# Kernel tuning notes

Measured on AMD Instinct MI355X. Metric: run time of the kernel, lower is better.

## Reference

```python
import jax, jax.numpy as jnp
import numpy as np

N, E, G = 100000, 1600000, 1024
F_IN, D, C = 1, 32, 10

def _lin(key, fin, fout):
    return jax.random.normal(key, (fin, fout), jnp.float32) / np.sqrt(fin)

def setup_inputs() -> dict:
    key = jax.random.key(0)
    ks = jax.random.split(key, 32)
    inp = {}
    inp['x'] = jax.random.normal(ks[0], (N, F_IN), jnp.float32)
    inp['edge_index'] = jax.random.randint(ks[1], (2, E), 0, N)
    inp['batch'] = jnp.sort(jax.random.randint(ks[2], (N,), 0, G))
    inp['num_graphs'] = G
    # conv1: ResGatedGraphConv(F_IN -> D)
    inp['c1_Wk'] = _lin(ks[3], F_IN, D); inp['c1_bk'] = jnp.zeros((D,), jnp.float32)
    inp['c1_Wq'] = _lin(ks[4], F_IN, D); inp['c1_bq'] = jnp.zeros((D,), jnp.float32)
    inp['c1_Wv'] = _lin(ks[5], F_IN, D); inp['c1_bv'] = jnp.zeros((D,), jnp.float32)
    inp['c1_Wskip'] = _lin(ks[6], F_IN, D); inp['c1_b'] = jnp.zeros((D,), jnp.float32)
    # conv2: FiLMConv(D -> D), num_relations=1
    inp['c2_Wlin'] = _lin(ks[7], D, D)
    inp['c2_Wfilm'] = _lin(ks[8], D, 2 * D); inp['c2_bfilm'] = jnp.zeros((2 * D,), jnp.float32)
    inp['c2_Wls'] = _lin(ks[9], D, D)
    inp['c2_Wfs'] = _lin(ks[10], D, 2 * D)
    # conv3: ResGatedGraphConv(D -> D)
    inp['c3_Wk'] = _lin(ks[11], D, D); inp['c3_bk'] = jnp.zeros((D,), jnp.float32)
    inp['c3_Wq'] = _lin(ks[12], D, D); inp['c3_bq'] = jnp.zeros((D,), jnp.float32)
    inp['c3_Wv'] = _lin(ks[13], D, D); inp['c3_bv'] = jnp.zeros((D,), jnp.float32)
    inp['c3_Wskip'] = _lin(ks[14], D, D); inp['c3_b'] = jnp.zeros((D,), jnp.float32)
    # final classifier
    inp['lin_W'] = _lin(ks[15], D, C); inp['lin_b'] = jnp.zeros((C,), jnp.float32)
    return inp

def _res_gated(x, src, dst, Wk, bk, Wq, bq, Wv, bv, Wskip, b):
    # out_i = sum_{j->i} sigmoid(k_i + q_j) * v_j + W_skip x_i + b
    k = x @ Wk + bk
    q = x @ Wq + bq
    v = x @ Wv + bv
    msg = jax.nn.sigmoid(k[dst] + q[src]) * v[src]  # [E, D]
    agg = jax.ops.segment_sum(msg, dst, num_segments=x.shape[0])
    return agg + x @ Wskip + b

def _film(x, src, dst, Wlin, Wfilm, bfilm, Wls, Wfs):
    # skip path: relu(gamma_skip * (W_skip x) + beta_skip)
    bg_s = x @ Wfs                       # [N, 2D]
    beta_s, gamma_s = jnp.split(bg_s, 2, axis=-1)
    out = jax.nn.relu(gamma_s * (x @ Wls) + beta_s)
    # message path: relu(gamma_i * (W x_j) + beta_i), mean aggregation
    bg = x @ Wfilm + bfilm
    beta, gamma = jnp.split(bg, 2, axis=-1)
    xl = x @ Wlin
    msg = jax.nn.relu(gamma[dst] * xl[src] + beta[dst])  # [E, D]
    sums = jax.ops.segment_sum(msg, dst, num_segments=x.shape[0])
    cnt = jax.ops.segment_sum(jnp.ones((dst.shape[0], 1), x.dtype), dst, num_segments=x.shape[0])
    return out + sums / jnp.maximum(cnt, 1.0)

def reference(x, edge_index, batch, num_graphs,
              c1_Wk, c1_bk, c1_Wq, c1_bq, c1_Wv, c1_bv, c1_Wskip, c1_b,
              c2_Wlin, c2_Wfilm, c2_bfilm, c2_Wls, c2_Wfs,
              c3_Wk, c3_bk, c3_Wq, c3_bq, c3_Wv, c3_bv, c3_Wskip, c3_b,
              lin_W, lin_b):
    src, dst = edge_index[0], edge_index[1]
    h = _res_gated(x, src, dst, c1_Wk, c1_bk, c1_Wq, c1_bq, c1_Wv, c1_bv, c1_Wskip, c1_b)
    h = jax.nn.relu(h)
    h = _film(h, src, dst, c2_Wlin, c2_Wfilm, c2_bfilm, c2_Wls, c2_Wfs)
    h = jax.nn.relu(h)
    h = _res_gated(h, src, dst, c3_Wk, c3_bk, c3_Wq, c3_bq, c3_Wv, c3_bv, c3_Wskip, c3_b)
    # global mean pool over graphs
    sums = jax.ops.segment_sum(h, batch, num_segments=num_graphs)
    cnt = jax.ops.segment_sum(jnp.ones((h.shape[0], 1), h.dtype), batch, num_segments=num_graphs)
    g = sums / jnp.maximum(cnt, 1.0)
    # dropout is identity in eval mode
    return g @ lin_W + lin_b
```

## Files before the change

kernel.cpp:

```cpp
#include <hip/hip_runtime.h>

#define N_NODES 100000
#define N_EDGES 1600000
#define N_GRAPH 1024
#define NB      196
#define BCAP    10240
#define PEPT    16

typedef unsigned short u16;
typedef unsigned int   u32;

__device__ __forceinline__ float sigm(float z) { return 1.0f / (1.0f + __expf(-z)); }
__device__ __forceinline__ u16 f2bf(float f) {
    u32 u = __float_as_uint(f);
    u += 0x7FFFu + ((u >> 16) & 1u);
    return (u16)(u >> 16);
}
__device__ __forceinline__ float bf2f(u16 h) { return __uint_as_float(((u32)h) << 16); }

__global__ __launch_bounds__(256) void k_partition(const int* __restrict__ ei,
                                                   int* __restrict__ gcnt,
                                                   int* __restrict__ bucketed)
{
    __shared__ int lcnt[NB], gbase[NB], lcur[NB];
    int t = threadIdx.x;
    for (int i = t; i < NB; i += 256) { lcnt[i] = 0; lcur[i] = 0; }
    __syncthreads();

    int ebase = blockIdx.x * (256 * PEPT);
    int pk[PEPT], bk[PEPT];
#pragma unroll
    for (int r = 0; r < PEPT; r++) {
        int e = ebase + r * 256 + t;
        if (e < N_EDGES) {
            int d = ei[N_EDGES + e];
            int s = ei[e];
            int b = d >> 9;
            bk[r] = b;
            pk[r] = ((d & 511) << 17) | s;
            atomicAdd(&lcnt[b], 1);
        } else bk[r] = -1;
    }
    __syncthreads();
    for (int i = t; i < NB; i += 256) gbase[i] = atomicAdd(&gcnt[i], lcnt[i]);
    __syncthreads();
#pragma unroll
    for (int r = 0; r < PEPT; r++) {
        if (bk[r] >= 0) {
            int b = bk[r];
            int pos = gbase[b] + atomicAdd(&lcur[b], 1);
            bucketed[b * BCAP + pos] = pk[r];
        }
    }
}

__global__ __launch_bounds__(256) void k_bscan(const int* __restrict__ gcnt,
                                               int* __restrict__ base)
{
    __shared__ int s[256];
    int t = threadIdx.x;
    int v = (t < NB) ? gcnt[t] : 0;
    s[t] = v;
    __syncthreads();
#pragma unroll
    for (int off = 1; off < 256; off <<= 1) {
        int u = (t >= off) ? s[t - off] : 0;
        __syncthreads();
        s[t] += u;
        __syncthreads();
    }
    base[t] = s[t] - v;
}

__global__ __launch_bounds__(512) void k_place(const int* __restrict__ bucketed,
                                               const int* __restrict__ gcnt,
                                               const int* __restrict__ base,
                                               int* __restrict__ csr,
                                               int* __restrict__ starts,
                                               int* __restrict__ cnt)
{
    __shared__ int scnt[512], sexc[512], scur[512];
    int b = blockIdx.x, t = threadIdx.x;
    int ecnt = gcnt[b];
    int ebase = base[b];
    const int* bp = bucketed + b * BCAP;

    scnt[t] = 0; scur[t] = 0;
    __syncthreads();
    for (int e = t; e < ecnt; e += 512) atomicAdd(&scnt[bp[e] >> 17], 1);
    __syncthreads();
    int v = scnt[t];
    sexc[t] = v;
    __syncthreads();
#pragma unroll
    for (int off = 1; off < 512; off <<= 1) {
        int u = (t >= off) ? sexc[t - off] : 0;
        __syncthreads();
        sexc[t] += u;
        __syncthreads();
    }
    int excl = sexc[t] - v;
    __syncthreads();
    sexc[t] = excl;
    __syncthreads();

    int node = b * 512 + t;
    if (node < N_NODES) { starts[node] = ebase + excl; cnt[node] = v; }

    for (int e = t; e < ecnt; e += 512) {
        int p = bp[e];
        int ld = p >> 17;
        int pos = ebase + sexc[ld] + atomicAdd(&scur[ld], 1);
        csr[pos] = p & 0x1FFFF;
    }
}

__global__ __launch_bounds__(256) void k_gath1(
    const float* __restrict__ x, const int* __restrict__ csr_src,
    const int* __restrict__ starts, const int* __restrict__ cnt,
    const float* __restrict__ Wk, const float* __restrict__ bk,
    const float* __restrict__ Wq, const float* __restrict__ bq,
    const float* __restrict__ Wv, const float* __restrict__ bv,
    const float* __restrict__ Wskip, const float* __restrict__ b,
    float* __restrict__ h1)
{
    int tid = blockIdx.x * 256 + threadIdx.x;
    if (tid >= N_NODES * 8) return;
    int i = tid >> 3, l = tid & 7;

    float xd = x[i];
    float4 wk = ((const float4*)Wk)[l], bk4 = ((const float4*)bk)[l];
    float4 wq = ((const float4*)Wq)[l], bq4 = ((const float4*)bq)[l];
    float4 wv = ((const float4*)Wv)[l], bv4 = ((const float4*)bv)[l];
    float4 kk = make_float4(fmaf(xd, wk.x, bk4.x), fmaf(xd, wk.y, bk4.y),
                            fmaf(xd, wk.z, bk4.z), fmaf(xd, wk.w, bk4.w));

    int base = starts[i], deg = cnt[i];
    float4 a0 = make_float4(0.f, 0.f, 0.f, 0.f);
    float4 a1 = make_float4(0.f, 0.f, 0.f, 0.f);
    int e = 0;
    for (; e + 1 < deg; e += 2) {
        int s0 = csr_src[base + e];
        int s1 = csr_src[base + e + 1];
        float x0 = x[s0], x1 = x[s1];
        a0.x += sigm(kk.x + fmaf(x0, wq.x, bq4.x)) * fmaf(x0, wv.x, bv4.x);
        a0.y += sigm(kk.y + fmaf(x0, wq.y, bq4.y)) * fmaf(x0, wv.y, bv4.y);
        a0.z += sigm(kk.z + fmaf(x0, wq.z, bq4.z)) * fmaf(x0, wv.z, bv4.z);
        a0.w += sigm(kk.w + fmaf(x0, wq.w, bq4.w)) * fmaf(x0, wv.w, bv4.w);
        a1.x += sigm(kk.x + fmaf(x1, wq.x, bq4.x)) * fmaf(x1, wv.x, bv4.x);
        a1.y += sigm(kk.y + fmaf(x1, wq.y, bq4.y)) * fmaf(x1, wv.y, bv4.y);
        a1.z += sigm(kk.z + fmaf(x1, wq.z, bq4.z)) * fmaf(x1, wv.z, bv4.z);
        a1.w += sigm(kk.w + fmaf(x1, wq.w, bq4.w)) * fmaf(x1, wv.w, bv4.w);
    }
    if (e < deg) {
        int s0 = csr_src[base + e];
        float x0 = x[s0];
        a0.x += sigm(kk.x + fmaf(x0, wq.x, bq4.x)) * fmaf(x0, wv.x, bv4.x);
        a0.y += sigm(kk.y + fmaf(x0, wq.y, bq4.y)) * fmaf(x0, wv.y, bv4.y);
        a0.z += sigm(kk.z + fmaf(x0, wq.z, bq4.z)) * fmaf(x0, wv.z, bv4.z);
        a0.w += sigm(kk.w + fmaf(x0, wq.w, bq4.w)) * fmaf(x0, wv.w, bv4.w);
    }
    float4 ws4 = ((const float4*)Wskip)[l];
    float4 bb4 = ((const float4*)b)[l];
    float4 o = make_float4(a0.x + a1.x + fmaf(xd, ws4.x, bb4.x),
                           a0.y + a1.y + fmaf(xd, ws4.y, bb4.y),
                           a0.z + a1.z + fmaf(xd, ws4.z, bb4.z),
                           a0.w + a1.w + fmaf(xd, ws4.w, bb4.w));
    ((float4*)(h1 + (size_t)i * 32))[l] = o;
}

__device__ __forceinline__ float4 dot4(const float* __restrict__ h,
                                       const float* __restrict__ Wcol, int stride)
{
    float4 a = make_float4(0.f, 0.f, 0.f, 0.f);
#pragma unroll
    for (int k = 0; k < 32; k++) {
        float4 w = *(const float4*)(Wcol + k * stride);
        float hk = h[k];
        a.x = fmaf(hk, w.x, a.x);
        a.y = fmaf(hk, w.y, a.y);
        a.z = fmaf(hk, w.z, a.z);
        a.w = fmaf(hk, w.w, a.w);
    }
    return a;
}

__global__ __launch_bounds__(256) void k_node2(
    const float* __restrict__ h1,
    const float* __restrict__ Wlin, const float* __restrict__ Wfilm,
    const float* __restrict__ bfilm, const float* __restrict__ Wls,
    const float* __restrict__ Wfs,
    float* __restrict__ skip2, float* __restrict__ bg2, u16* __restrict__ xlb)
{
    __shared__ float sWlin[32 * 32], sWfilm[32 * 64], sWls[32 * 32], sWfs[32 * 64];
    int t = threadIdx.x;
    for (int idx = t; idx < 1024; idx += 256) sWlin[idx] = Wlin[idx];
    for (int idx = t; idx < 2048; idx += 256) sWfilm[idx] = Wfilm[idx];
    for (int idx = t; idx < 1024; idx += 256) sWls[idx] = Wls[idx];
    for (int idx = t; idx < 2048; idx += 256) sWfs[idx] = Wfs[idx];
    __syncthreads();

    int tid = blockIdx.x * 256 + t;
    if (tid >= N_NODES * 8) return;
    int i = tid >> 3, l = tid & 7;

    float h[32];
    const float4* hp = (const float4*)(h1 + (size_t)i * 32);
#pragma unroll
    for (int j = 0; j < 8; j++) {
        float4 v = hp[j];
        h[4 * j + 0] = fmaxf(v.x, 0.f);
        h[4 * j + 1] = fmaxf(v.y, 0.f);
        h[4 * j + 2] = fmaxf(v.z, 0.f);
        h[4 * j + 3] = fmaxf(v.w, 0.f);
    }

    float4 bs = dot4(h, sWfs + l * 4, 64);
    float4 gs = dot4(h, sWfs + 32 + l * 4, 64);
    float4 ls = dot4(h, sWls + l * 4, 32);
    float4 sk = make_float4(fmaxf(fmaf(gs.x, ls.x, bs.x), 0.f),
                            fmaxf(fmaf(gs.y, ls.y, bs.y), 0.f),
                            fmaxf(fmaf(gs.z, ls.z, bs.z), 0.f),
                            fmaxf(fmaf(gs.w, ls.w, bs.w), 0.f));
    ((float4*)(skip2 + (size_t)i * 32))[l] = sk;

    float4 bf0 = ((const float4*)bfilm)[l * 2];
    float4 bf1 = ((const float4*)bfilm)[l * 2 + 1];
    float4 f0 = dot4(h, sWfilm + l * 8, 64);
    float4 f1 = dot4(h, sWfilm + l * 8 + 4, 64);
    f0.x += bf0.x; f0.y += bf0.y; f0.z += bf0.z; f0.w += bf0.w;
    f1.x += bf1.x; f1.y += bf1.y; f1.z += bf1.z; f1.w += bf1.w;
    float4* bgp = (float4*)(bg2 + (size_t)i * 64);
    bgp[l * 2] = f0;
    bgp[l * 2 + 1] = f1;

    float4 xo = dot4(h, sWlin + l * 4, 32);
    ushort4 xp;
    xp.x = f2bf(xo.x); xp.y = f2bf(xo.y); xp.z = f2bf(xo.z); xp.w = f2bf(xo.w);
    ((ushort4*)xlb)[(size_t)i * 8 + l] = xp;
}

__global__ __launch_bounds__(256) void k_gath2(
    const int* __restrict__ csr_src, const int* __restrict__ starts,
    const int* __restrict__ cnt,
    const float* __restrict__ bg2, const u16* __restrict__ xlb,
    const float* __restrict__ skip2, float* __restrict__ h2)
{
    int tid = blockIdx.x * 256 + threadIdx.x;
    if (tid >= N_NODES * 8) return;
    int i = tid >> 3, l = tid & 7;

    float4 be = ((const float4*)(bg2 + (size_t)i * 64))[l];
    float4 ga = ((const float4*)(bg2 + (size_t)i * 64 + 32))[l];

    int base = starts[i], deg = cnt[i];
    float4 a0 = make_float4(0.f, 0.f, 0.f, 0.f);
    float4 a1 = make_float4(0.f, 0.f, 0.f, 0.f);
    int e = 0;
    for (; e + 1 < deg; e += 2) {
        int s0 = csr_src[base + e];
        int s1 = csr_src[base + e + 1];
        ushort4 u = ((const ushort4*)xlb)[(size_t)s0 * 8 + l];
        ushort4 w = ((const ushort4*)xlb)[(size_t)s1 * 8 + l];
        a0.x += fmaxf(fmaf(ga.x, bf2f(u.x), be.x), 0.f);
        a0.y += fmaxf(fmaf(ga.y, bf2f(u.y), be.y), 0.f);
        a0.z += fmaxf(fmaf(ga.z, bf2f(u.z), be.z), 0.f);
        a0.w += fmaxf(fmaf(ga.w, bf2f(u.w), be.w), 0.f);
        a1.x += fmaxf(fmaf(ga.x, bf2f(w.x), be.x), 0.f);
        a1.y += fmaxf(fmaf(ga.y, bf2f(w.y), be.y), 0.f);
        a1.z += fmaxf(fmaf(ga.z, bf2f(w.z), be.z), 0.f);
        a1.w += fmaxf(fmaf(ga.w, bf2f(w.w), be.w), 0.f);
    }
    if (e < deg) {
        int s0 = csr_src[base + e];
        ushort4 u = ((const ushort4*)xlb)[(size_t)s0 * 8 + l];
        a0.x += fmaxf(fmaf(ga.x, bf2f(u.x), be.x), 0.f);
        a0.y += fmaxf(fmaf(ga.y, bf2f(u.y), be.y), 0.f);
        a0.z += fmaxf(fmaf(ga.z, bf2f(u.z), be.z), 0.f);
        a0.w += fmaxf(fmaf(ga.w, bf2f(u.w), be.w), 0.f);
    }
    float inv = 1.0f / fmaxf((float)deg, 1.0f);
    float4 sk = ((const float4*)(skip2 + (size_t)i * 32))[l];
    float4 o = make_float4(fmaxf(fmaf(a0.x + a1.x, inv, sk.x), 0.f),
                           fmaxf(fmaf(a0.y + a1.y, inv, sk.y), 0.f),
                           fmaxf(fmaf(a0.z + a1.z, inv, sk.z), 0.f),
                           fmaxf(fmaf(a0.w + a1.w, inv, sk.w), 0.f));
    ((float4*)(h2 + (size_t)i * 32))[l] = o;
}

__global__ __launch_bounds__(256) void k_node3(
    const float* __restrict__ h2,
    const float* __restrict__ Wk, const float* __restrict__ bk,
    const float* __restrict__ Wq, const float* __restrict__ bq,
    const float* __restrict__ Wv, const float* __restrict__ bv,
    const float* __restrict__ Wskip, const float* __restrict__ b,
    float* __restrict__ k3, u16* __restrict__ qvb, float* __restrict__ acc3)
{
    __shared__ float sWk[1024], sWq[1024], sWv[1024], sWs[1024];
    int t = threadIdx.x;
    for (int idx = t; idx < 1024; idx += 256) {
        sWk[idx] = Wk[idx];
        sWq[idx] = Wq[idx];
        sWv[idx] = Wv[idx];
        sWs[idx] = Wskip[idx];
    }
    __syncthreads();

    int tid = blockIdx.x * 256 + t;
    if (tid >= N_NODES * 8) return;
    int i = tid >> 3, l = tid & 7;

    float h[32];
    const float4* hp = (const float4*)(h2 + (size_t)i * 32);
#pragma unroll
    for (int j = 0; j < 8; j++) {
        float4 v = hp[j];
        h[4 * j + 0] = v.x; h[4 * j + 1] = v.y;
        h[4 * j + 2] = v.z; h[4 * j + 3] = v.w;
    }

    float4 bk4 = ((const float4*)bk)[l];
    float4 bq4 = ((const float4*)bq)[l];
    float4 bv4 = ((const float4*)bv)[l];
    float4 bb4 = ((const float4*)b)[l];

    float4 kk = dot4(h, sWk + l * 4, 32);
    kk.x += bk4.x; kk.y += bk4.y; kk.z += bk4.z; kk.w += bk4.w;
    ((float4*)(k3 + (size_t)i * 32))[l] = kk;

    float4 qq = dot4(h, sWq + l * 4, 32);
    qq.x += bq4.x; qq.y += bq4.y; qq.z += bq4.z; qq.w += bq4.w;
    float4 vv = dot4(h, sWv + l * 4, 32);
    vv.x += bv4.x; vv.y += bv4.y; vv.z += bv4.z; vv.w += bv4.w;

    uint4 pk;
    pk.x = (u32)f2bf(qq.x) | ((u32)f2bf(qq.y) << 16);
    pk.y = (u32)f2bf(qq.z) | ((u32)f2bf(qq.w) << 16);
    pk.z = (u32)f2bf(vv.x) | ((u32)f2bf(vv.y) << 16);
    pk.w = (u32)f2bf(vv.z) | ((u32)f2bf(vv.w) << 16);
    ((uint4*)qvb)[(size_t)i * 8 + l] = pk;

    float4 ss = dot4(h, sWs + l * 4, 32);
    ss.x += bb4.x; ss.y += bb4.y; ss.z += bb4.z; ss.w += bb4.w;
    ((float4*)(acc3 + (size_t)i * 32))[l] = ss;
}

__global__ __launch_bounds__(256) void k_gath3(
    const int* __restrict__ csr_src, const int* __restrict__ starts,
    const int* __restrict__ cnt,
    const float* __restrict__ k3, const u16* __restrict__ qvb,
    float* __restrict__ acc3)
{
    int tid = blockIdx.x * 256 + threadIdx.x;
    if (tid >= N_NODES * 8) return;
    int i = tid >> 3, l = tid & 7;

    float4 kk = ((const float4*)(k3 + (size_t)i * 32))[l];
    int base = starts[i], deg = cnt[i];
    float4 a0 = make_float4(0.f, 0.f, 0.f, 0.f);
    float4 a1 = make_float4(0.f, 0.f, 0.f, 0.f);
    int e = 0;
    for (; e + 1 < deg; e += 2) {
        int s0 = csr_src[base + e];
        int s1 = csr_src[base + e + 1];
        uint4 p0 = ((const uint4*)qvb)[(size_t)s0 * 8 + l];
        uint4 p1 = ((const uint4*)qvb)[(size_t)s1 * 8 + l];
        a0.x += sigm(kk.x + bf2f((u16)p0.x)) * bf2f((u16)p0.z);
        a0.y += sigm(kk.y + bf2f((u16)(p0.x >> 16))) * bf2f((u16)(p0.z >> 16));
        a0.z += sigm(kk.z + bf2f((u16)p0.y)) * bf2f((u16)p0.w);
        a0.w += sigm(kk.w + bf2f((u16)(p0.y >> 16))) * bf2f((u16)(p0.w >> 16));
        a1.x += sigm(kk.x + bf2f((u16)p1.x)) * bf2f((u16)p1.z);
        a1.y += sigm(kk.y + bf2f((u16)(p1.x >> 16))) * bf2f((u16)(p1.z >> 16));
        a1.z += sigm(kk.z + bf2f((u16)p1.y)) * bf2f((u16)p1.w);
        a1.w += sigm(kk.w + bf2f((u16)(p1.y >> 16))) * bf2f((u16)(p1.w >> 16));
    }
    if (e < deg) {
        int s0 = csr_src[base + e];
        uint4 p0 = ((const uint4*)qvb)[(size_t)s0 * 8 + l];
        a0.x += sigm(kk.x + bf2f((u16)p0.x)) * bf2f((u16)p0.z);
        a0.y += sigm(kk.y + bf2f((u16)(p0.x >> 16))) * bf2f((u16)(p0.z >> 16));
        a0.z += sigm(kk.z + bf2f((u16)p0.y)) * bf2f((u16)p0.w);
        a0.w += sigm(kk.w + bf2f((u16)(p0.y >> 16))) * bf2f((u16)(p0.w >> 16));
    }
    float4* op = (float4*)(acc3 + (size_t)i * 32) + l;
    float4 cur = *op;
    cur.x += a0.x + a1.x;
    cur.y += a0.y + a1.y;
    cur.z += a0.z + a1.z;
    cur.w += a0.w + a1.w;
    *op = cur;
}

__global__ __launch_bounds__(256) void k_gstart(const int* __restrict__ batch,
                                                int* __restrict__ gstart)
{
    int g = blockIdx.x * 256 + threadIdx.x;
    if (g > N_GRAPH) return;
    int lo = 0, hi = N_NODES;
    while (lo < hi) {
        int mid = (lo + hi) >> 1;
        if (batch[mid] < g) lo = mid + 1; else hi = mid;
    }
    gstart[g] = lo;
}

__global__ __launch_bounds__(256) void k_pool(
    const float* __restrict__ h3, const int* __restrict__ gstart,
    float* __restrict__ gmean)
{
    int tid = blockIdx.x * 256 + threadIdx.x;
    int g = tid >> 6;
    if (g >= N_GRAPH) return;
    int lane = tid & 63;
    int sub = lane >> 3, fg = lane & 7;
    int gs = gstart[g], ge = gstart[g + 1];

    float4 a = make_float4(0.f, 0.f, 0.f, 0.f);
    for (int j = gs + sub; j < ge; j += 8) {
        float4 v = ((const float4*)(h3 + (size_t)j * 32))[fg];
        a.x += v.x; a.y += v.y; a.z += v.z; a.w += v.w;
    }
#pragma unroll
    for (int off = 8; off < 64; off <<= 1) {
        a.x += __shfl_xor(a.x, off);
        a.y += __shfl_xor(a.y, off);
        a.z += __shfl_xor(a.z, off);
        a.w += __shfl_xor(a.w, off);
    }
    if (sub == 0) {
        float inv = 1.0f / fmaxf((float)(ge - gs), 1.0f);
        a.x *= inv; a.y *= inv; a.z *= inv; a.w *= inv;
        ((float4*)(gmean + (size_t)g * 32))[fg] = a;
    }
}

__global__ __launch_bounds__(256) void k_final(
    const float* __restrict__ gmean,
    const float* __restrict__ linW, const float* __restrict__ linb,
    float* __restrict__ out)
{
    int tid = blockIdx.x * 256 + threadIdx.x;
    if (tid >= N_GRAPH * 10) return;
    int g = tid / 10, c = tid % 10;
    const float* gr = gmean + (size_t)g * 32;
    float a = 0.f;
#pragma unroll
    for (int k = 0; k < 32; k++) a = fmaf(gr[k], linW[k * 10 + c], a);
    out[tid] = a + linb[c];
}

extern "C" void kernel_launch(void* const* d_in, const int* in_sizes, int n_in,
                              void* d_out, int out_size, void* d_ws, size_t ws_size,
                              hipStream_t stream)
{
    const float* x      = (const float*)d_in[0];
    const int*   ei     = (const int*)d_in[1];
    const int*   batch  = (const int*)d_in[2];
    const float* c1_Wk   = (const float*)d_in[4];
    const float* c1_bk   = (const float*)d_in[5];
    const float* c1_Wq   = (const float*)d_in[6];
    const float* c1_bq   = (const float*)d_in[7];
    const float* c1_Wv   = (const float*)d_in[8];
    const float* c1_bv   = (const float*)d_in[9];
    const float* c1_Wsk  = (const float*)d_in[10];
    const float* c1_b    = (const float*)d_in[11];
    const float* c2_Wlin = (const float*)d_in[12];
    const float* c2_Wfilm= (const float*)d_in[13];
    const float* c2_bfilm= (const float*)d_in[14];
    const float* c2_Wls  = (const float*)d_in[15];
    const float* c2_Wfs  = (const float*)d_in[16];
    const float* c3_Wk   = (const float*)d_in[17];
    const float* c3_bk   = (const float*)d_in[18];
    const float* c3_Wq   = (const float*)d_in[19];
    const float* c3_bq   = (const float*)d_in[20];
    const float* c3_Wv   = (const float*)d_in[21];
    const float* c3_bv   = (const float*)d_in[22];
    const float* c3_Wsk  = (const float*)d_in[23];
    const float* c3_b    = (const float*)d_in[24];
    const float* lin_W   = (const float*)d_in[25];
    const float* lin_b   = (const float*)d_in[26];
    float* out = (float*)d_out;

    const size_t N = N_NODES;

    int* gcnt    = (int*)d_ws;
    int* bbase   = gcnt + 256;
    int* igstart = bbase + 256;
    int* bucketed= igstart + 1056;
    int* icsr    = bucketed + NB * BCAP;
    int* istarts = icsr + N_EDGES;
    int* icnt    = istarts + N;
    float* fbase = (float*)(icnt + N);
    float* h1    = fbase;
    float* skip2 = h1 + N * 32;
    float* bg2   = skip2 + N * 32;
    u16*   xlb   = (u16*)(bg2 + N * 64);
    float* gmean = (float*)(xlb + N * 32);

    hipMemsetAsync(gcnt, 0, 256 * sizeof(int), stream);

    const int TB = 256;
    int gPart  = (N_EDGES + 256 * PEPT - 1) / (256 * PEPT);
    int gNode8 = (N_NODES * 8 + TB - 1) / TB;
    int gFin   = (N_GRAPH * 10 + TB - 1) / TB;

    k_partition<<<gPart, TB, 0, stream>>>(ei, gcnt, bucketed);
    k_bscan<<<1, 256, 0, stream>>>(gcnt, bbase);
    k_place<<<NB, 512, 0, stream>>>(bucketed, gcnt, bbase, icsr, istarts, icnt);
    k_gstart<<<5, TB, 0, stream>>>(batch, igstart);

    k_gath1<<<gNode8, TB, 0, stream>>>(x, icsr, istarts, icnt,
                                       c1_Wk, c1_bk, c1_Wq, c1_bq,
                                       c1_Wv, c1_bv, c1_Wsk, c1_b, h1);
    k_node2<<<gNode8, TB, 0, stream>>>(h1, c2_Wlin, c2_Wfilm, c2_bfilm,
                                       c2_Wls, c2_Wfs, skip2, bg2, xlb);
    float* h2 = h1;
    k_gath2<<<gNode8, TB, 0, stream>>>(icsr, istarts, icnt, bg2, xlb, skip2, h2);
    float* k3   = skip2;
    u16*   qvb  = (u16*)bg2;
    float* acc3 = bg2 + N * 32;
    k_node3<<<gNode8, TB, 0, stream>>>(h2, c3_Wk, c3_bk, c3_Wq, c3_bq,
                                       c3_Wv, c3_bv, c3_Wsk, c3_b,
                                       k3, qvb, acc3);
    k_gath3<<<gNode8, TB, 0, stream>>>(icsr, istarts, icnt, k3, qvb, acc3);
    k_pool<<<256, TB, 0, stream>>>(acc3, igstart, gmean);
    k_final<<<gFin, TB, 0, stream>>>(gmean, lin_W, lin_b, out);
}
```

Measured before the change: 338.4 us.

## Fuse per-node transforms into gather kernels and degree-sort node processing order

Splits the node-wise transforms so that only the source-side projections (xl, q/v) are precomputed. The destination-side projections (FiLM beta/gamma, skip, k) are now computed inside the gather kernels, which removes writing and re-reading the skip2, bg2, k3 and acc3 intermediates. It also builds a per-block degree-binned permutation in k_place so the gather kernels process nodes grouped by similar degree, which reduces divergence within a wavefront. The cost is recomputing small matvecs inside the gathers, extra shared-memory weight loads per block, and an indirection through perm that scatters the per-node reads and writes.

```diff
diff --git a/kernel.cpp b/kernel.cpp
--- a/kernel.cpp
+++ b/kernel.cpp
@@ -77,9 +77,10 @@
                                                const int* __restrict__ base,
                                                int* __restrict__ csr,
                                                int* __restrict__ starts,
-                                               int* __restrict__ cnt)
-{
-    __shared__ int scnt[512], sexc[512], scur[512];
+                                               int* __restrict__ cnt,
+                                               int* __restrict__ perm)
+{
+    __shared__ int scnt[512], sexc[512], scur[512], dbin[64];
     int b = blockIdx.x, t = threadIdx.x;
     int ecnt = gcnt[b];
     int ebase = base[b];
@@ -113,11 +114,30 @@
         int pos = ebase + sexc[ld] + atomicAdd(&scur[ld], 1);
         csr[pos] = p & 0x1FFFF;
     }
+
+    __syncthreads();
+    if (t < 64) dbin[t] = 0;
+    __syncthreads();
+    int nvalid = N_NODES - b * 512;
+    if (nvalid > 512) nvalid = 512;
+    int mybin = (t < nvalid) ? (v < 63 ? v : 63) : -1;
+    if (mybin >= 0) atomicAdd(&dbin[mybin], 1);
+    __syncthreads();
+    if (t == 0) {
+        int acc = 0;
+        for (int i = 0; i < 64; i++) { int c = dbin[i]; dbin[i] = acc; acc += c; }
+    }
+    __syncthreads();
+    if (mybin >= 0) {
+        int pos = atomicAdd(&dbin[mybin], 1);
+        perm[b * 512 + pos] = node;
+    }
 }
 
 __global__ __launch_bounds__(256) void k_gath1(
     const float* __restrict__ x, const int* __restrict__ csr_src,
     const int* __restrict__ starts, const int* __restrict__ cnt,
+    const int* __restrict__ perm,
     const float* __restrict__ Wk, const float* __restrict__ bk,
     const float* __restrict__ Wq, const float* __restrict__ bq,
     const float* __restrict__ Wv, const float* __restrict__ bv,
@@ -126,7 +146,7 @@
 {
     int tid = blockIdx.x * 256 + threadIdx.x;
     if (tid >= N_NODES * 8) return;
-    int i = tid >> 3, l = tid & 7;
+    int i = perm[tid >> 3], l = tid & 7;
 
     float xd = x[i];
     float4 wk = ((const float4*)Wk)[l], bk4 = ((const float4*)bk)[l];
@@ -185,16 +205,45 @@
     return a;
 }
 
-__global__ __launch_bounds__(256) void k_node2(
-    const float* __restrict__ h1,
-    const float* __restrict__ Wlin, const float* __restrict__ Wfilm,
-    const float* __restrict__ bfilm, const float* __restrict__ Wls,
-    const float* __restrict__ Wfs,
-    float* __restrict__ skip2, float* __restrict__ bg2, u16* __restrict__ xlb)
-{
-    __shared__ float sWlin[32 * 32], sWfilm[32 * 64], sWls[32 * 32], sWfs[32 * 64];
+__global__ __launch_bounds__(256) void k_xl(
+    const float* __restrict__ h1, const float* __restrict__ Wlin,
+    u16* __restrict__ xlb)
+{
+    __shared__ float sWlin[1024];
     int t = threadIdx.x;
     for (int idx = t; idx < 1024; idx += 256) sWlin[idx] = Wlin[idx];
+    __syncthreads();
+
+    int tid = blockIdx.x * 256 + t;
+    if (tid >= N_NODES * 8) return;
+    int i = tid >> 3, l = tid & 7;
+
+    float h[32];
+    const float4* hp = (const float4*)(h1 + (size_t)i * 32);
+#pragma unroll
+    for (int j = 0; j < 8; j++) {
+        float4 v = hp[j];
+        h[4 * j + 0] = fmaxf(v.x, 0.f);
+        h[4 * j + 1] = fmaxf(v.y, 0.f);
+        h[4 * j + 2] = fmaxf(v.z, 0.f);
+        h[4 * j + 3] = fmaxf(v.w, 0.f);
+    }
+    float4 xo = dot4(h, sWlin + l * 4, 32);
+    ushort4 xp;
+    xp.x = f2bf(xo.x); xp.y = f2bf(xo.y); xp.z = f2bf(xo.z); xp.w = f2bf(xo.w);
+    ((ushort4*)xlb)[(size_t)i * 8 + l] = xp;
+}
+
+__global__ __launch_bounds__(256) void k_gath2f(
+    const int* __restrict__ csr_src, const int* __restrict__ starts,
+    const int* __restrict__ cnt, const int* __restrict__ perm,
+    const float* __restrict__ h1, const u16* __restrict__ xlb,
+    const float* __restrict__ Wfilm, const float* __restrict__ bfilm,
+    const float* __restrict__ Wls, const float* __restrict__ Wfs,
+    float* __restrict__ h2)
+{
+    __shared__ float sWfilm[2048], sWls[1024], sWfs[2048];
+    int t = threadIdx.x;
     for (int idx = t; idx < 2048; idx += 256) sWfilm[idx] = Wfilm[idx];
     for (int idx = t; idx < 1024; idx += 256) sWls[idx] = Wls[idx];
     for (int idx = t; idx < 2048; idx += 256) sWfs[idx] = Wfs[idx];
@@ -202,7 +251,7 @@
 
     int tid = blockIdx.x * 256 + t;
     if (tid >= N_NODES * 8) return;
-    int i = tid >> 3, l = tid & 7;
+    int i = perm[tid >> 3], l = tid & 7;
 
     float h[32];
     const float4* hp = (const float4*)(h1 + (size_t)i * 32);
@@ -222,36 +271,13 @@
                             fmaxf(fmaf(gs.y, ls.y, bs.y), 0.f),
                             fmaxf(fmaf(gs.z, ls.z, bs.z), 0.f),
                             fmaxf(fmaf(gs.w, ls.w, bs.w), 0.f));
-    ((float4*)(skip2 + (size_t)i * 32))[l] = sk;
-
-    float4 bf0 = ((const float4*)bfilm)[l * 2];
-    float4 bf1 = ((const float4*)bfilm)[l * 2 + 1];
-    float4 f0 = dot4(h, sWfilm + l * 8, 64);
-    float4 f1 = dot4(h, sWfilm + l * 8 + 4, 64);
-    f0.x += bf0.x; f0.y += bf0.y; f0.z += bf0.z; f0.w += bf0.w;
-    f1.x += bf1.x; f1.y += bf1.y; f1.z += bf1.z; f1.w += bf1.w;
-    float4* bgp = (float4*)(bg2 + (size_t)i * 64);
-    bgp[l * 2] = f0;
-    bgp[l * 2 + 1] = f1;
-
-    float4 xo = dot4(h, sWlin + l * 4, 32);
-    ushort4 xp;
-    xp.x = f2bf(xo.x); xp.y = f2bf(xo.y); xp.z = f2bf(xo.z); xp.w = f2bf(xo.w);
-    ((ushort4*)xlb)[(size_t)i * 8 + l] = xp;
-}
-
-__global__ __launch_bounds__(256) void k_gath2(
-    const int* __restrict__ csr_src, const int* __restrict__ starts,
-    const int* __restrict__ cnt,
-    const float* __restrict__ bg2, const u16* __restrict__ xlb,
-    const float* __restrict__ skip2, float* __restrict__ h2)
-{
-    int tid = blockIdx.x * 256 + threadIdx.x;
-    if (tid >= N_NODES * 8) return;
-    int i = tid >> 3, l = tid & 7;
-
-    float4 be = ((const float4*)(bg2 + (size_t)i * 64))[l];
-    float4 ga = ((const float4*)(bg2 + (size_t)i * 64 + 32))[l];
+
+    float4 bf = ((const float4*)bfilm)[l];
+    float4 gf = ((const float4*)bfilm)[8 + l];
+    float4 be = dot4(h, sWfilm + l * 4, 64);
+    float4 ga = dot4(h, sWfilm + 32 + l * 4, 64);
+    be.x += bf.x; be.y += bf.y; be.z += bf.z; be.w += bf.w;
+    ga.x += gf.x; ga.y += gf.y; ga.z += gf.z; ga.w += gf.w;
 
     int base = starts[i], deg = cnt[i];
     float4 a0 = make_float4(0.f, 0.f, 0.f, 0.f);
@@ -280,7 +306,6 @@
         a0.w += fmaxf(fmaf(ga.w, bf2f(u.w), be.w), 0.f);
     }
     float inv = 1.0f / fmaxf((float)deg, 1.0f);
-    float4 sk = ((const float4*)(skip2 + (size_t)i * 32))[l];
     float4 o = make_float4(fmaxf(fmaf(a0.x + a1.x, inv, sk.x), 0.f),
                            fmaxf(fmaf(a0.y + a1.y, inv, sk.y), 0.f),
                            fmaxf(fmaf(a0.z + a1.z, inv, sk.z), 0.f),
@@ -288,22 +313,15 @@
     ((float4*)(h2 + (size_t)i * 32))[l] = o;
 }
 
-__global__ __launch_bounds__(256) void k_node3(
+__global__ __launch_bounds__(256) void k_qv(
     const float* __restrict__ h2,
-    const float* __restrict__ Wk, const float* __restrict__ bk,
     const float* __restrict__ Wq, const float* __restrict__ bq,
     const float* __restrict__ Wv, const float* __restrict__ bv,
-    const float* __restrict__ Wskip, const float* __restrict__ b,
-    float* __restrict__ k3, u16* __restrict__ qvb, float* __restrict__ acc3)
-{
-    __shared__ float sWk[1024], sWq[1024], sWv[1024], sWs[1024];
+    u16* __restrict__ qvb)
+{
+    __shared__ float sWq[1024], sWv[1024];
     int t = threadIdx.x;
-    for (int idx = t; idx < 1024; idx += 256) {
-        sWk[idx] = Wk[idx];
-        sWq[idx] = Wq[idx];
-        sWv[idx] = Wv[idx];
-        sWs[idx] = Wskip[idx];
-    }
+    for (int idx = t; idx < 1024; idx += 256) { sWq[idx] = Wq[idx]; sWv[idx] = Wv[idx]; }
     __syncthreads();
 
     int tid = blockIdx.x * 256 + t;
@@ -318,16 +336,8 @@
         h[4 * j + 0] = v.x; h[4 * j + 1] = v.y;
         h[4 * j + 2] = v.z; h[4 * j + 3] = v.w;
     }
-
-    float4 bk4 = ((const float4*)bk)[l];
     float4 bq4 = ((const float4*)bq)[l];
     float4 bv4 = ((const float4*)bv)[l];
-    float4 bb4 = ((const float4*)b)[l];
-
-    float4 kk = dot4(h, sWk + l * 4, 32);
-    kk.x += bk4.x; kk.y += bk4.y; kk.z += bk4.z; kk.w += bk4.w;
-    ((float4*)(k3 + (size_t)i * 32))[l] = kk;
-
     float4 qq = dot4(h, sWq + l * 4, 32);
     qq.x += bq4.x; qq.y += bq4.y; qq.z += bq4.z; qq.w += bq4.w;
     float4 vv = dot4(h, sWv + l * 4, 32);
@@ -339,23 +349,40 @@
     pk.z = (u32)f2bf(vv.x) | ((u32)f2bf(vv.y) << 16);
     pk.w = (u32)f2bf(vv.z) | ((u32)f2bf(vv.w) << 16);
     ((uint4*)qvb)[(size_t)i * 8 + l] = pk;
-
+}
+
+__global__ __launch_bounds__(256) void k_gath3f(
+    const int* __restrict__ csr_src, const int* __restrict__ starts,
+    const int* __restrict__ cnt, const int* __restrict__ perm,
+    const float* __restrict__ h2, const u16* __restrict__ qvb,
+    const float* __restrict__ Wk, const float* __restrict__ bk,
+    const float* __restrict__ Wskip, const float* __restrict__ b,
+    float* __restrict__ h3)
+{
+    __shared__ float sWk[1024], sWs[1024];
+    int t = threadIdx.x;
+    for (int idx = t; idx < 1024; idx += 256) { sWk[idx] = Wk[idx]; sWs[idx] = Wskip[idx]; }
+    __syncthreads();
+
+    int tid = blockIdx.x * 256 + t;
+    if (tid >= N_NODES * 8) return;
+    int i = perm[tid >> 3], l = tid & 7;
+
+    float h[32];
+    const float4* hp = (const float4*)(h2 + (size_t)i * 32);
+#pragma unroll
+    for (int j = 0; j < 8; j++) {
+        float4 v = hp[j];
+        h[4 * j + 0] = v.x; h[4 * j + 1] = v.y;
+        h[4 * j + 2] = v.z; h[4 * j + 3] = v.w;
+    }
+    float4 bk4 = ((const float4*)bk)[l];
+    float4 bb4 = ((const float4*)b)[l];
+    float4 kk = dot4(h, sWk + l * 4, 32);
+    kk.x += bk4.x; kk.y += bk4.y; kk.z += bk4.z; kk.w += bk4.w;
     float4 ss = dot4(h, sWs + l * 4, 32);
     ss.x += bb4.x; ss.y += bb4.y; ss.z += bb4.z; ss.w += bb4.w;
-    ((float4*)(acc3 + (size_t)i * 32))[l] = ss;
-}
-
-__global__ __launch_bounds__(256) void k_gath3(
-    const int* __restrict__ csr_src, const int* __restrict__ starts,
-    const int* __restrict__ cnt,
-    const float* __restrict__ k3, const u16* __restrict__ qvb,
-    float* __restrict__ acc3)
-{
-    int tid = blockIdx.x * 256 + threadIdx.x;
-    if (tid >= N_NODES * 8) return;
-    int i = tid >> 3, l = tid & 7;
-
-    float4 kk = ((const float4*)(k3 + (size_t)i * 32))[l];
+
     int base = starts[i], deg = cnt[i];
     float4 a0 = make_float4(0.f, 0.f, 0.f, 0.f);
     float4 a1 = make_float4(0.f, 0.f, 0.f, 0.f);
@@ -382,13 +409,9 @@
         a0.z += sigm(kk.z + bf2f((u16)p0.y)) * bf2f((u16)p0.w);
         a0.w += sigm(kk.w + bf2f((u16)(p0.y >> 16))) * bf2f((u16)(p0.w >> 16));
     }
-    float4* op = (float4*)(acc3 + (size_t)i * 32) + l;
-    float4 cur = *op;
-    cur.x += a0.x + a1.x;
-    cur.y += a0.y + a1.y;
-    cur.z += a0.z + a1.z;
-    cur.w += a0.w + a1.w;
-    *op = cur;
+    float4 o = make_float4(ss.x + a0.x + a1.x, ss.y + a0.y + a1.y,
+                           ss.z + a0.z + a1.z, ss.w + a0.w + a1.w);
+    ((float4*)(h3 + (size_t)i * 32))[l] = o;
 }
 
 __global__ __launch_bounds__(256) void k_gstart(const int* __restrict__ batch,
@@ -490,12 +513,12 @@
     int* icsr    = bucketed + NB * BCAP;
     int* istarts = icsr + N_EDGES;
     int* icnt    = istarts + N;
-    float* fbase = (float*)(icnt + N);
-    float* h1    = fbase;
-    float* skip2 = h1 + N * 32;
-    float* bg2   = skip2 + N * 32;
-    u16*   xlb   = (u16*)(bg2 + N * 64);
-    float* gmean = (float*)(xlb + N * 32);
+    int* iperm   = icnt + N;
+    float* h1    = (float*)(iperm + N);
+    float* h2    = h1 + N * 32;
+    u16*   xlb   = (u16*)(h2 + N * 32);
+    u16*   qvb   = xlb + N * 32;
+    float* gmean = (float*)(qvb + N * 64);
 
     hipMemsetAsync(gcnt, 0, 256 * sizeof(int), stream);
 
@@ -506,23 +529,19 @@
 
     k_partition<<<gPart, TB, 0, stream>>>(ei, gcnt, bucketed);
     k_bscan<<<1, 256, 0, stream>>>(gcnt, bbase);
-    k_place<<<NB, 512, 0, stream>>>(bucketed, gcnt, bbase, icsr, istarts, icnt);
+    k_place<<<NB, 512, 0, stream>>>(bucketed, gcnt, bbase, icsr, istarts, icnt, iperm);
     k_gstart<<<5, TB, 0, stream>>>(batch, igstart);
 
-    k_gath1<<<gNode8, TB, 0, stream>>>(x, icsr, istarts, icnt,
+    k_gath1<<<gNode8, TB, 0, stream>>>(x, icsr, istarts, icnt, iperm,
                                        c1_Wk, c1_bk, c1_Wq, c1_bq,
                                        c1_Wv, c1_bv, c1_Wsk, c1_b, h1);
-    k_node2<<<gNode8, TB, 0, stream>>>(h1, c2_Wlin, c2_Wfilm, c2_bfilm,
-                                       c2_Wls, c2_Wfs, skip2, bg2, xlb);
-    float* h2 = h1;
-    k_gath2<<<gNode8, TB, 0, stream>>>(icsr, istarts, icnt, bg2, xlb, skip2, h2);
-    float* k3   = skip2;
-    u16*   qvb  = (u16*)bg2;
-    float* acc3 = bg2 + N * 32;
-    k_node3<<<gNode8, TB, 0, stream>>>(h2, c3_Wk, c3_bk, c3_Wq, c3_bq,
-                                       c3_Wv, c3_bv, c3_Wsk, c3_b,
-                                       k3, qvb, acc3);
-    k_gath3<<<gNode8, TB, 0, stream>>>(icsr, istarts, icnt, k3, qvb, acc3);
-    k_pool<<<256, TB, 0, stream>>>(acc3, igstart, gmean);
+    k_xl<<<gNode8, TB, 0, stream>>>(h1, c2_Wlin, xlb);
+    k_gath2f<<<gNode8, TB, 0, stream>>>(icsr, istarts, icnt, iperm, h1, xlb,
+                                        c2_Wfilm, c2_bfilm, c2_Wls, c2_Wfs, h2);
+    k_qv<<<gNode8, TB, 0, stream>>>(h2, c3_Wq, c3_bq, c3_Wv, c3_bv, qvb);
+    float* h3 = h1;
+    k_gath3f<<<gNode8, TB, 0, stream>>>(icsr, istarts, icnt, iperm, h2, qvb,
+                                        c3_Wk, c3_bk, c3_Wsk, c3_b, h3);
+    k_pool<<<256, TB, 0, stream>>>(h3, igstart, gmean);
     k_final<<<gFin, TB, 0, stream>>>(gmean, lin_W, lin_b, out);
 }
```

Result: slower. 510.4 us (+50.8%).

## Factor sigmoid into per-node exponentials and unroll gather loops by four

Applied to the files above, without the earlier changes.

Rewrites sigmoid(k_i+q_j) as 1/(1+exp(-k_i)*exp(-q_j)), so the exponentials are computed once per node and each edge costs only an FMA plus a hardware reciprocal. A new pre-kernel for layer 1 precomputes packed bf16 exp(-q) and v per node, and layer 3's node kernel now stores exp(-k) and exp(-q). The gather loops in all three layers are unrolled to four edges to keep more loads in flight. In exchange there is an extra kernel launch, layer 1 now reads 16-byte bf16 rows per edge instead of a scalar x, and exp(-q) in bf16 can overflow or lose precision for large activations.

```diff
diff --git a/kernel.cpp b/kernel.cpp
--- a/kernel.cpp
+++ b/kernel.cpp
@@ -10,13 +10,13 @@
 typedef unsigned short u16;
 typedef unsigned int   u32;
 
-__device__ __forceinline__ float sigm(float z) { return 1.0f / (1.0f + __expf(-z)); }
 __device__ __forceinline__ u16 f2bf(float f) {
     u32 u = __float_as_uint(f);
     u += 0x7FFFu + ((u >> 16) & 1u);
     return (u16)(u >> 16);
 }
 __device__ __forceinline__ float bf2f(u16 h) { return __uint_as_float(((u32)h) << 16); }
+__device__ __forceinline__ float rcpf(float x) { return __builtin_amdgcn_rcpf(x); }
 
 __global__ __launch_bounds__(256) void k_partition(const int* __restrict__ ei,
                                                    int* __restrict__ gcnt,
@@ -115,12 +115,45 @@
     }
 }
 
+__global__ __launch_bounds__(256) void k_pre1(
+    const float* __restrict__ x,
+    const float* __restrict__ Wq, const float* __restrict__ bq,
+    const float* __restrict__ Wv, const float* __restrict__ bv,
+    u32* __restrict__ eqv1)
+{
+    int tid = blockIdx.x * 256 + threadIdx.x;
+    if (tid >= N_NODES * 8) return;
+    int i = tid >> 3, l = tid & 7;
+    float xv = x[i];
+    float4 wq = ((const float4*)Wq)[l], bq4 = ((const float4*)bq)[l];
+    float4 wv = ((const float4*)Wv)[l], bv4 = ((const float4*)bv)[l];
+    float e0 = __expf(-fmaf(xv, wq.x, bq4.x));
+    float e1 = __expf(-fmaf(xv, wq.y, bq4.y));
+    float e2 = __expf(-fmaf(xv, wq.z, bq4.z));
+    float e3 = __expf(-fmaf(xv, wq.w, bq4.w));
+    float v0 = fmaf(xv, wv.x, bv4.x);
+    float v1 = fmaf(xv, wv.y, bv4.y);
+    float v2 = fmaf(xv, wv.z, bv4.z);
+    float v3 = fmaf(xv, wv.w, bv4.w);
+    uint4 pk;
+    pk.x = (u32)f2bf(e0) | ((u32)f2bf(e1) << 16);
+    pk.y = (u32)f2bf(e2) | ((u32)f2bf(e3) << 16);
+    pk.z = (u32)f2bf(v0) | ((u32)f2bf(v1) << 16);
+    pk.w = (u32)f2bf(v2) | ((u32)f2bf(v3) << 16);
+    ((uint4*)eqv1)[(size_t)i * 8 + l] = pk;
+}
+
+#define EDGE_ACC(P, ACC)                                                        \
+    ACC.x += bf2f((u16)(P.z)) * rcpf(fmaf(ek.x, bf2f((u16)(P.x)), 1.0f));       \
+    ACC.y += bf2f((u16)(P.z >> 16)) * rcpf(fmaf(ek.y, bf2f((u16)(P.x >> 16)), 1.0f)); \
+    ACC.z += bf2f((u16)(P.w)) * rcpf(fmaf(ek.z, bf2f((u16)(P.y)), 1.0f));       \
+    ACC.w += bf2f((u16)(P.w >> 16)) * rcpf(fmaf(ek.w, bf2f((u16)(P.y >> 16)), 1.0f));
+
 __global__ __launch_bounds__(256) void k_gath1(
     const float* __restrict__ x, const int* __restrict__ csr_src,
     const int* __restrict__ starts, const int* __restrict__ cnt,
+    const u32* __restrict__ eqv1,
     const float* __restrict__ Wk, const float* __restrict__ bk,
-    const float* __restrict__ Wq, const float* __restrict__ bq,
-    const float* __restrict__ Wv, const float* __restrict__ bv,
     const float* __restrict__ Wskip, const float* __restrict__ b,
     float* __restrict__ h1)
 {
@@ -130,35 +163,32 @@
 
     float xd = x[i];
     float4 wk = ((const float4*)Wk)[l], bk4 = ((const float4*)bk)[l];
-    float4 wq = ((const float4*)Wq)[l], bq4 = ((const float4*)bq)[l];
-    float4 wv = ((const float4*)Wv)[l], bv4 = ((const float4*)bv)[l];
-    float4 kk = make_float4(fmaf(xd, wk.x, bk4.x), fmaf(xd, wk.y, bk4.y),
-                            fmaf(xd, wk.z, bk4.z), fmaf(xd, wk.w, bk4.w));
+    float4 ek;
+    ek.x = __expf(-fmaf(xd, wk.x, bk4.x));
+    ek.y = __expf(-fmaf(xd, wk.y, bk4.y));
+    ek.z = __expf(-fmaf(xd, wk.z, bk4.z));
+    ek.w = __expf(-fmaf(xd, wk.w, bk4.w));
 
     int base = starts[i], deg = cnt[i];
+    const uint4* qv = (const uint4*)eqv1;
     float4 a0 = make_float4(0.f, 0.f, 0.f, 0.f);
     float4 a1 = make_float4(0.f, 0.f, 0.f, 0.f);
     int e = 0;
-    for (; e + 1 < deg; e += 2) {
+    for (; e + 3 < deg; e += 4) {
         int s0 = csr_src[base + e];
         int s1 = csr_src[base + e + 1];
-        float x0 = x[s0], x1 = x[s1];
-        a0.x += sigm(kk.x + fmaf(x0, wq.x, bq4.x)) * fmaf(x0, wv.x, bv4.x);
-        a0.y += sigm(kk.y + fmaf(x0, wq.y, bq4.y)) * fmaf(x0, wv.y, bv4.y);
-        a0.z += sigm(kk.z + fmaf(x0, wq.z, bq4.z)) * fmaf(x0, wv.z, bv4.z);
-        a0.w += sigm(kk.w + fmaf(x0, wq.w, bq4.w)) * fmaf(x0, wv.w, bv4.w);
-        a1.x += sigm(kk.x + fmaf(x1, wq.x, bq4.x)) * fmaf(x1, wv.x, bv4.x);
-        a1.y += sigm(kk.y + fmaf(x1, wq.y, bq4.y)) * fmaf(x1, wv.y, bv4.y);
-        a1.z += sigm(kk.z + fmaf(x1, wq.z, bq4.z)) * fmaf(x1, wv.z, bv4.z);
-        a1.w += sigm(kk.w + fmaf(x1, wq.w, bq4.w)) * fmaf(x1, wv.w, bv4.w);
-    }
-    if (e < deg) {
+        int s2 = csr_src[base + e + 2];
+        int s3 = csr_src[base + e + 3];
+        uint4 p0 = qv[(size_t)s0 * 8 + l];
+        uint4 p1 = qv[(size_t)s1 * 8 + l];
+        uint4 p2 = qv[(size_t)s2 * 8 + l];
+        uint4 p3 = qv[(size_t)s3 * 8 + l];
+        EDGE_ACC(p0, a0) EDGE_ACC(p1, a1) EDGE_ACC(p2, a0) EDGE_ACC(p3, a1)
+    }
+    for (; e < deg; e++) {
         int s0 = csr_src[base + e];
-        float x0 = x[s0];
-        a0.x += sigm(kk.x + fmaf(x0, wq.x, bq4.x)) * fmaf(x0, wv.x, bv4.x);
-        a0.y += sigm(kk.y + fmaf(x0, wq.y, bq4.y)) * fmaf(x0, wv.y, bv4.y);
-        a0.z += sigm(kk.z + fmaf(x0, wq.z, bq4.z)) * fmaf(x0, wv.z, bv4.z);
-        a0.w += sigm(kk.w + fmaf(x0, wq.w, bq4.w)) * fmaf(x0, wv.w, bv4.w);
+        uint4 p0 = qv[(size_t)s0 * 8 + l];
+        EDGE_ACC(p0, a0)
     }
     float4 ws4 = ((const float4*)Wskip)[l];
     float4 bb4 = ((const float4*)b)[l];
@@ -192,7 +222,7 @@
     const float* __restrict__ Wfs,
     float* __restrict__ skip2, float* __restrict__ bg2, u16* __restrict__ xlb)
 {
-    __shared__ float sWlin[32 * 32], sWfilm[32 * 64], sWls[32 * 32], sWfs[32 * 64];
+    __shared__ float sWlin[1024], sWfilm[2048], sWls[1024], sWfs[2048];
     int t = threadIdx.x;
     for (int idx = t; idx < 1024; idx += 256) sWlin[idx] = Wlin[idx];
     for (int idx = t; idx < 2048; idx += 256) sWfilm[idx] = Wfilm[idx];
@@ -240,6 +270,12 @@
     ((ushort4*)xlb)[(size_t)i * 8 + l] = xp;
 }
 
+#define EDGE_ACC2(U, ACC)                                   \
+    ACC.x += fmaxf(fmaf(ga.x, bf2f(U.x), be.x), 0.f);       \
+    ACC.y += fmaxf(fmaf(ga.y, bf2f(U.y), be.y), 0.f);       \
+    ACC.z += fmaxf(fmaf(ga.z, bf2f(U.z), be.z), 0.f);       \
+    ACC.w += fmaxf(fmaf(ga.w, bf2f(U.w), be.w), 0.f);
+
 __global__ __launch_bounds__(256) void k_gath2(
     const int* __restrict__ csr_src, const int* __restrict__ starts,
     const int* __restrict__ cnt,
@@ -254,32 +290,27 @@
     float4 ga = ((const float4*)(bg2 + (size_t)i * 64 + 32))[l];
 
     int base = starts[i], deg = cnt[i];
+    const ushort4* xp = (const ushort4*)xlb;
     float4 a0 = make_float4(0.f, 0.f, 0.f, 0.f);
     float4 a1 = make_float4(0.f, 0.f, 0.f, 0.f);
     int e = 0;
-    for (; e + 1 < deg; e += 2) {
+    for (; e + 3 < deg; e += 4) {
         int s0 = csr_src[base + e];
         int s1 = csr_src[base + e + 1];
-        ushort4 u = ((const ushort4*)xlb)[(size_t)s0 * 8 + l];
-        ushort4 w = ((const ushort4*)xlb)[(size_t)s1 * 8 + l];
-        a0.x += fmaxf(fmaf(ga.x, bf2f(u.x), be.x), 0.f);
-        a0.y += fmaxf(fmaf(ga.y, bf2f(u.y), be.y), 0.f);
-        a0.z += fmaxf(fmaf(ga.z, bf2f(u.z), be.z), 0.f);
-        a0.w += fmaxf(fmaf(ga.w, bf2f(u.w), be.w), 0.f);
-        a1.x += fmaxf(fmaf(ga.x, bf2f(w.x), be.x), 0.f);
-        a1.y += fmaxf(fmaf(ga.y, bf2f(w.y), be.y), 0.f);
-        a1.z += fmaxf(fmaf(ga.z, bf2f(w.z), be.z), 0.f);
-        a1.w += fmaxf(fmaf(ga.w, bf2f(w.w), be.w), 0.f);
-    }
-    if (e < deg) {
+        int s2 = csr_src[base + e + 2];
+        int s3 = csr_src[base + e + 3];
+        ushort4 u0 = xp[(size_t)s0 * 8 + l];
+        ushort4 u1 = xp[(size_t)s1 * 8 + l];
+        ushort4 u2 = xp[(size_t)s2 * 8 + l];
+        ushort4 u3 = xp[(size_t)s3 * 8 + l];
+        EDGE_ACC2(u0, a0) EDGE_ACC2(u1, a1) EDGE_ACC2(u2, a0) EDGE_ACC2(u3, a1)
+    }
+    for (; e < deg; e++) {
         int s0 = csr_src[base + e];
-        ushort4 u = ((const ushort4*)xlb)[(size_t)s0 * 8 + l];
-        a0.x += fmaxf(fmaf(ga.x, bf2f(u.x), be.x), 0.f);
-        a0.y += fmaxf(fmaf(ga.y, bf2f(u.y), be.y), 0.f);
-        a0.z += fmaxf(fmaf(ga.z, bf2f(u.z), be.z), 0.f);
-        a0.w += fmaxf(fmaf(ga.w, bf2f(u.w), be.w), 0.f);
-    }
-    float inv = 1.0f / fmaxf((float)deg, 1.0f);
+        ushort4 u0 = xp[(size_t)s0 * 8 + l];
+        EDGE_ACC2(u0, a0)
+    }
+    float inv = rcpf(fmaxf((float)deg, 1.0f));
     float4 sk = ((const float4*)(skip2 + (size_t)i * 32))[l];
     float4 o = make_float4(fmaxf(fmaf(a0.x + a1.x, inv, sk.x), 0.f),
                            fmaxf(fmaf(a0.y + a1.y, inv, sk.y), 0.f),
@@ -294,7 +325,7 @@
     const float* __restrict__ Wq, const float* __restrict__ bq,
     const float* __restrict__ Wv, const float* __restrict__ bv,
     const float* __restrict__ Wskip, const float* __restrict__ b,
-    float* __restrict__ k3, u16* __restrict__ qvb, float* __restrict__ acc3)
+    float* __restrict__ ek3, u32* __restrict__ qvb, float* __restrict__ acc3)
 {
     __shared__ float sWk[1024], sWq[1024], sWv[1024], sWs[1024];
     int t = threadIdx.x;
@@ -325,17 +356,24 @@
     float4 bb4 = ((const float4*)b)[l];
 
     float4 kk = dot4(h, sWk + l * 4, 32);
-    kk.x += bk4.x; kk.y += bk4.y; kk.z += bk4.z; kk.w += bk4.w;
-    ((float4*)(k3 + (size_t)i * 32))[l] = kk;
+    float4 ekv;
+    ekv.x = __expf(-(kk.x + bk4.x));
+    ekv.y = __expf(-(kk.y + bk4.y));
+    ekv.z = __expf(-(kk.z + bk4.z));
+    ekv.w = __expf(-(kk.w + bk4.w));
+    ((float4*)(ek3 + (size_t)i * 32))[l] = ekv;
 
     float4 qq = dot4(h, sWq + l * 4, 32);
-    qq.x += bq4.x; qq.y += bq4.y; qq.z += bq4.z; qq.w += bq4.w;
     float4 vv = dot4(h, sWv + l * 4, 32);
+    float eq0 = __expf(-(qq.x + bq4.x));
+    float eq1 = __expf(-(qq.y + bq4.y));
+    float eq2 = __expf(-(qq.z + bq4.z));
+    float eq3 = __expf(-(qq.w + bq4.w));
     vv.x += bv4.x; vv.y += bv4.y; vv.z += bv4.z; vv.w += bv4.w;
 
     uint4 pk;
-    pk.x = (u32)f2bf(qq.x) | ((u32)f2bf(qq.y) << 16);
-    pk.y = (u32)f2bf(qq.z) | ((u32)f2bf(qq.w) << 16);
+    pk.x = (u32)f2bf(eq0) | ((u32)f2bf(eq1) << 16);
+    pk.y = (u32)f2bf(eq2) | ((u32)f2bf(eq3) << 16);
     pk.z = (u32)f2bf(vv.x) | ((u32)f2bf(vv.y) << 16);
     pk.w = (u32)f2bf(vv.z) | ((u32)f2bf(vv.w) << 16);
     ((uint4*)qvb)[(size_t)i * 8 + l] = pk;
@@ -348,39 +386,34 @@
 __global__ __launch_bounds__(256) void k_gath3(
     const int* __restrict__ csr_src, const int* __restrict__ starts,
     const int* __restrict__ cnt,
-    const float* __restrict__ k3, const u16* __restrict__ qvb,
+    const float* __restrict__ ek3, const u32* __restrict__ qvb,
     float* __restrict__ acc3)
 {
     int tid = blockIdx.x * 256 + threadIdx.x;
     if (tid >= N_NODES * 8) return;
     int i = tid >> 3, l = tid & 7;
 
-    float4 kk = ((const float4*)(k3 + (size_t)i * 32))[l];
+    float4 ek = ((const float4*)(ek3 + (size_t)i * 32))[l];
     int base = starts[i], deg = cnt[i];
+    const uint4* qv = (const uint4*)qvb;
     float4 a0 = make_float4(0.f, 0.f, 0.f, 0.f);
     float4 a1 = make_float4(0.f, 0.f, 0.f, 0.f);
     int e = 0;
-    for (; e + 1 < deg; e += 2) {
+    for (; e + 3 < deg; e += 4) {
         int s0 = csr_src[base + e];
         int s1 = csr_src[base + e + 1];
-        uint4 p0 = ((const uint4*)qvb)[(size_t)s0 * 8 + l];
-        uint4 p1 = ((const uint4*)qvb)[(size_t)s1 * 8 + l];
-        a0.x += sigm(kk.x + bf2f((u16)p0.x)) * bf2f((u16)p0.z);
-        a0.y += sigm(kk.y + bf2f((u16)(p0.x >> 16))) * bf2f((u16)(p0.z >> 16));
-        a0.z += sigm(kk.z + bf2f((u16)p0.y)) * bf2f((u16)p0.w);
-        a0.w += sigm(kk.w + bf2f((u16)(p0.y >> 16))) * bf2f((u16)(p0.w >> 16));
-        a1.x += sigm(kk.x + bf2f((u16)p1.x)) * bf2f((u16)p1.z);
-        a1.y += sigm(kk.y + bf2f((u16)(p1.x >> 16))) * bf2f((u16)(p1.z >> 16));
-        a1.z += sigm(kk.z + bf2f((u16)p1.y)) * bf2f((u16)p1.w);
-        a1.w += sigm(kk.w + bf2f((u16)(p1.y >> 16))) * bf2f((u16)(p1.w >> 16));
-    }
-    if (e < deg) {
+        int s2 = csr_src[base + e + 2];
+        int s3 = csr_src[base + e + 3];
+        uint4 p0 = qv[(size_t)s0 * 8 + l];
+        uint4 p1 = qv[(size_t)s1 * 8 + l];
+        uint4 p2 = qv[(size_t)s2 * 8 + l];
+        uint4 p3 = qv[(size_t)s3 * 8 + l];
+        EDGE_ACC(p0, a0) EDGE_ACC(p1, a1) EDGE_ACC(p2, a0) EDGE_ACC(p3, a1)
+    }
+    for (; e < deg; e++) {
         int s0 = csr_src[base + e];
-        uint4 p0 = ((const uint4*)qvb)[(size_t)s0 * 8 + l];
-        a0.x += sigm(kk.x + bf2f((u16)p0.x)) * bf2f((u16)p0.z);
-        a0.y += sigm(kk.y + bf2f((u16)(p0.x >> 16))) * bf2f((u16)(p0.z >> 16));
-        a0.z += sigm(kk.z + bf2f((u16)p0.y)) * bf2f((u16)p0.w);
-        a0.w += sigm(kk.w + bf2f((u16)(p0.y >> 16))) * bf2f((u16)(p0.w >> 16));
+        uint4 p0 = qv[(size_t)s0 * 8 + l];
+        EDGE_ACC(p0, a0)
     }
     float4* op = (float4*)(acc3 + (size_t)i * 32) + l;
     float4 cur = *op;
@@ -490,12 +523,12 @@
     int* icsr    = bucketed + NB * BCAP;
     int* istarts = icsr + N_EDGES;
     int* icnt    = istarts + N;
-    float* fbase = (float*)(icnt + N);
-    float* h1    = fbase;
+    float* h1    = (float*)(icnt + N);
     float* skip2 = h1 + N * 32;
     float* bg2   = skip2 + N * 32;
     u16*   xlb   = (u16*)(bg2 + N * 64);
-    float* gmean = (float*)(xlb + N * 32);
+    u32*   eqv1  = (u32*)(xlb + N * 32);
+    float* gmean = (float*)(eqv1 + N * 32);
 
     hipMemsetAsync(gcnt, 0, 256 * sizeof(int), stream);
 
@@ -509,20 +542,20 @@
     k_place<<<NB, 512, 0, stream>>>(bucketed, gcnt, bbase, icsr, istarts, icnt);
     k_gstart<<<5, TB, 0, stream>>>(batch, igstart);
 
-    k_gath1<<<gNode8, TB, 0, stream>>>(x, icsr, istarts, icnt,
-                                       c1_Wk, c1_bk, c1_Wq, c1_bq,
-                                       c1_Wv, c1_bv, c1_Wsk, c1_b, h1);
+    k_pre1<<<gNode8, TB, 0, stream>>>(x, c1_Wq, c1_bq, c1_Wv, c1_bv, eqv1);
+    k_gath1<<<gNode8, TB, 0, stream>>>(x, icsr, istarts, icnt, eqv1,
+                                       c1_Wk, c1_bk, c1_Wsk, c1_b, h1);
     k_node2<<<gNode8, TB, 0, stream>>>(h1, c2_Wlin, c2_Wfilm, c2_bfilm,
                                        c2_Wls, c2_Wfs, skip2, bg2, xlb);
     float* h2 = h1;
     k_gath2<<<gNode8, TB, 0, stream>>>(icsr, istarts, icnt, bg2, xlb, skip2, h2);
-    float* k3   = skip2;
-    u16*   qvb  = (u16*)bg2;
+    float* ek3  = skip2;
+    u32*   qvb  = (u32*)bg2;
     float* acc3 = bg2 + N * 32;
     k_node3<<<gNode8, TB, 0, stream>>>(h2, c3_Wk, c3_bk, c3_Wq, c3_bq,
                                        c3_Wv, c3_bv, c3_Wsk, c3_b,
-                                       k3, qvb, acc3);
-    k_gath3<<<gNode8, TB, 0, stream>>>(icsr, istarts, icnt, k3, qvb, acc3);
+                                       ek3, qvb, acc3);
+    k_gath3<<<gNode8, TB, 0, stream>>>(icsr, istarts, icnt, ek3, qvb, acc3);
     k_pool<<<256, TB, 0, stream>>>(acc3, igstart, gmean);
     k_final<<<gFin, TB, 0, stream>>>(gmean, lin_W, lin_b, out);
 }
```

After: 313.4 us. -7.4%, faster.
